# Kernel optimization log

Hardware: AMD Instinct MI355X
Metric: run time of the kernel (lower is better)

Reference implementation:

```python
import jax, jax.numpy as jnp
import numpy as np

DIM = 128
N_NODES = 50000
N_EDGES = 625000


def setup_inputs() -> dict:
    key = jax.random.key(0)
    ks = jax.random.split(key, 6)
    X = jax.random.normal(ks[0], (N_NODES, DIM), dtype=jnp.float32)
    edge_index = jax.random.randint(ks[1], (2, N_EDGES), 0, N_NODES, dtype=jnp.int64)
    # Linear params, init like torch (uniform +/- 1/sqrt(dim))
    bound = 1.0 / np.sqrt(DIM)
    msg_w = jax.random.uniform(ks[2], (DIM, DIM), minval=-bound, maxval=bound, dtype=jnp.float32)
    msg_b = jax.random.uniform(ks[3], (DIM,), minval=-bound, maxval=bound, dtype=jnp.float32)
    lin_w = jax.random.uniform(ks[4], (DIM, DIM), minval=-bound, maxval=bound, dtype=jnp.float32)
    lin_b = jax.random.uniform(ks[5], (DIM,), minval=-bound, maxval=bound, dtype=jnp.float32)
    eps = jnp.asarray(0.0, dtype=jnp.float32)
    return {"X": X, "edge_index": edge_index, "eps": eps,
            "msg_w": msg_w, "msg_b": msg_b, "lin_w": lin_w, "lin_b": lin_b}


def reference(X, edge_index, eps, msg_w, msg_b, lin_w, lin_b):
    src, dst = edge_index[0], edge_index[1]
    # msg_lin(X) then gather at dst: (E, F)
    msg = (jnp.einsum('nf,gf->ng', X, msg_w) + msg_b)[dst]
    # scatter-add messages onto src nodes: (N, F)
    agg = jax.ops.segment_sum(msg, src, num_segments=X.shape[0])
    out = (1.0 + eps) * X + agg
    out = jnp.einsum('nf,gf->ng', out, lin_w) + lin_b
    return jax.nn.relu(out)
```

## Files before the change

### kernel.cpp

```cpp
#include <hip/hip_runtime.h>
#include <hip/hip_bf16.h>

#define NN 50000
#define NE 625000
#define DIM 128

#define NBKT 782
#define NBKTP 784
#define CAP 1536
#define CHUNK 4096
#define NCHUNK ((NE + CHUNK - 1) / CHUNK)

using fragAB = __attribute__((ext_vector_type(8))) short;
using fragC  = __attribute__((ext_vector_type(4))) float;

__device__ __forceinline__ unsigned short f2bf(float f) {
    unsigned int u = __float_as_uint(f);
    unsigned int r = u + 0x7FFFu + ((u >> 16) & 1u);
    return (unsigned short)(r >> 16);
}

__device__ __forceinline__ float bflo(unsigned v) { return __uint_as_float(v << 16); }
__device__ __forceinline__ float bfhi(unsigned v) { return __uint_as_float(v & 0xffff0000u); }

__global__ void prep_kernel(const float* __restrict__ L, const float* __restrict__ W,
                            const float* __restrict__ mb, float* __restrict__ cb,
                            unsigned short* __restrict__ Bh) {
    int idx = blockIdx.x * 256 + threadIdx.x;
    if (idx < DIM * DIM) {
        int o = idx >> 7, g = idx & 127;
        float s = 0.f;
        for (int f = 0; f < DIM; f++) s += L[o * DIM + f] * W[f * DIM + g];
        Bh[o * 256 + 128 + g] = f2bf(s);
        Bh[o * 256 + g] = f2bf(L[o * DIM + g]);
    } else if (idx < DIM * DIM + DIM) {
        int o = idx - DIM * DIM;
        float s = 0.f;
        for (int f = 0; f < DIM; f++) s += L[o * DIM + f] * mb[f];
        cb[o] = s;
    }
}

__global__ __launch_bounds__(256) void xcast_kernel(const float* __restrict__ X,
                                                    unsigned short* __restrict__ Ah) {
    int idx = (blockIdx.x * 256 + threadIdx.x) * 4;
    if (idx >= NN * DIM) return;
    int n = idx >> 7, k = idx & 127;
    float4 v = *(const float4*)(X + idx);
    uint2 p;
    p.x = (unsigned int)f2bf(v.x) | ((unsigned int)f2bf(v.y) << 16);
    p.y = (unsigned int)f2bf(v.z) | ((unsigned int)f2bf(v.w) << 16);
    *(uint2*)(Ah + (size_t)n * 256 + k) = p;
}

__global__ __launch_bounds__(256) void bin_kernel(const int* __restrict__ ei,
                                                  int* __restrict__ bucket_cursor,
                                                  unsigned* __restrict__ staging) {
    __shared__ int cnt[NBKTP];
    __shared__ int base[NBKTP];
    __shared__ int gb[NBKTP];
    __shared__ int sarr[256];
    __shared__ unsigned staged[CHUNK];
    int t = threadIdx.x;
    int e0 = blockIdx.x * CHUNK;
    int nthis = NE - e0; if (nthis > CHUNK) nthis = CHUNK;

    for (int i = t; i < NBKTP; i += 256) cnt[i] = 0;
    __syncthreads();

    unsigned pk[16];
#pragma unroll
    for (int i = 0; i < 16; i++) {
        int e = e0 + i * 256 + t;
        if (e < NE) {
            int s = ei[e];
            int d = ei[NE + e];
            unsigned b = (unsigned)s >> 6;
            pk[i] = (b << 22) | ((unsigned)(s & 63) << 16) | (unsigned)d;
            atomicAdd(&cnt[b], 1);
        } else pk[i] = 0xFFFFFFFFu;
    }
    __syncthreads();

    int myb = t * 4;
    int s0 = 0;
    if (myb < NBKTP) s0 = cnt[myb] + cnt[myb + 1] + cnt[myb + 2] + cnt[myb + 3];
    sarr[t] = s0;
    __syncthreads();
    for (int off = 1; off < 256; off <<= 1) {
        int v = (t >= off) ? sarr[t - off] : 0;
        __syncthreads();
        sarr[t] += v;
        __syncthreads();
    }
    int run = sarr[t] - s0;
    if (myb < NBKTP) {
        for (int i = 0; i < 4; i++) {
            int b = myb + i;
            base[b] = run;
            int c = cnt[b];
            gb[b] = (b < NBKT && c > 0) ? atomicAdd(&bucket_cursor[b], c) : 0;
            run += c;
        }
    }
    __syncthreads();
    if (myb < NBKTP) {
        for (int i = 0; i < 4; i++) cnt[myb + i] = base[myb + i];
    }
    __syncthreads();

#pragma unroll
    for (int i = 0; i < 16; i++) {
        if (pk[i] != 0xFFFFFFFFu) {
            unsigned b = pk[i] >> 22;
            int pos = atomicAdd(&cnt[b], 1);
            staged[pos] = pk[i];
        }
    }
    __syncthreads();

    for (int idx = t; idx < nthis; idx += 256) {
        unsigned p = staged[idx];
        unsigned b = p >> 22;
        int pos = gb[b] + (idx - base[b]);
        if (pos < CAP) staging[(size_t)b * CAP + pos] = p;
    }
}

__global__ __launch_bounds__(256) void bucket_scan(const int* __restrict__ bucket_cursor,
                                                   int* __restrict__ bucket_base) {
    __shared__ int s[256];
    int t = threadIdx.x;
    int myb = t * 4;
    int v[4]; int s0 = 0;
#pragma unroll
    for (int i = 0; i < 4; i++) {
        int b = myb + i;
        int c = (b < NBKT) ? bucket_cursor[b] : 0;
        if (c > CAP) c = CAP;
        v[i] = c; s0 += c;
    }
    s[t] = s0;
    __syncthreads();
    for (int off = 1; off < 256; off <<= 1) {
        int u = (t >= off) ? s[t - off] : 0;
        __syncthreads();
        s[t] += u;
        __syncthreads();
    }
    int run = s[t] - s0;
#pragma unroll
    for (int i = 0; i < 4; i++) {
        int b = myb + i;
        if (b < NBKT) bucket_base[b] = run;
        run += v[i];
    }
}

__global__ __launch_bounds__(256) void bucket_sort(const int* __restrict__ bucket_cursor,
                                                   const int* __restrict__ bucket_base,
                                                   const unsigned* __restrict__ staging,
                                                   int* __restrict__ deg, int* __restrict__ offs,
                                                   int* __restrict__ sdst) {
    __shared__ unsigned rec[CAP];
    __shared__ unsigned sorted_[CAP];
    __shared__ int hcnt[64];
    __shared__ int hbase[64];
    __shared__ int cur[64];
    int t = threadIdx.x;
    int b = blockIdx.x;
    int cnt_b = bucket_cursor[b];
    if (cnt_b > CAP) cnt_b = CAP;
    int base_b = bucket_base[b];

    if (t < 64) hcnt[t] = 0;
    __syncthreads();
    for (int i = t; i < cnt_b; i += 256) {
        unsigned r = staging[(size_t)b * CAP + i];
        rec[i] = r;
        atomicAdd(&hcnt[(r >> 16) & 63], 1);
    }
    __syncthreads();
    if (t == 0) {
        int run = 0;
        for (int i = 0; i < 64; i++) { hbase[i] = run; run += hcnt[i]; }
    }
    __syncthreads();
    if (t < 64) {
        cur[t] = hbase[t];
        int src = b * 64 + t;
        if (src < NN) {
            deg[src] = hcnt[t];
            offs[src] = base_b + hbase[t];
        }
    }
    __syncthreads();
    for (int i = t; i < cnt_b; i += 256) {
        unsigned r = rec[i];
        int pos = atomicAdd(&cur[(r >> 16) & 63], 1);
        sorted_[pos] = r;
    }
    __syncthreads();
    for (int i = t; i < cnt_b; i += 256)
        sdst[base_b + i] = (int)(sorted_[i] & 0xFFFFu);
}

__global__ __launch_bounds__(256) void gather_kernel(const int* __restrict__ offs,
                                                     const int* __restrict__ deg,
                                                     const int* __restrict__ sdst,
                                                     unsigned short* Ah) {
    int wave = (blockIdx.x * 256 + threadIdx.x) >> 6;
    int lane = threadIdx.x & 63;
    if (wave >= NN) return;
    int start = __builtin_amdgcn_readfirstlane(offs[wave]);
    int cnt = __builtin_amdgcn_readfirstlane(deg[wave]);
    const unsigned* __restrict__ Ad = (const unsigned*)Ah;
    float ax = 0.f, ay = 0.f;
    int j = 0;
    for (; j + 8 <= cnt; j += 8) {
        int d0 = sdst[start + j + 0];
        int d1 = sdst[start + j + 1];
        int d2 = sdst[start + j + 2];
        int d3 = sdst[start + j + 3];
        int d4 = sdst[start + j + 4];
        int d5 = sdst[start + j + 5];
        int d6 = sdst[start + j + 6];
        int d7 = sdst[start + j + 7];
        unsigned v0 = Ad[(size_t)d0 * 128 + lane];
        unsigned v1 = Ad[(size_t)d1 * 128 + lane];
        unsigned v2 = Ad[(size_t)d2 * 128 + lane];
        unsigned v3 = Ad[(size_t)d3 * 128 + lane];
        unsigned v4 = Ad[(size_t)d4 * 128 + lane];
        unsigned v5 = Ad[(size_t)d5 * 128 + lane];
        unsigned v6 = Ad[(size_t)d6 * 128 + lane];
        unsigned v7 = Ad[(size_t)d7 * 128 + lane];
        ax += bflo(v0) + bflo(v1) + bflo(v2) + bflo(v3) +
              bflo(v4) + bflo(v5) + bflo(v6) + bflo(v7);
        ay += bfhi(v0) + bfhi(v1) + bfhi(v2) + bfhi(v3) +
              bfhi(v4) + bfhi(v5) + bfhi(v6) + bfhi(v7);
    }
    if (j + 4 <= cnt) {
        int d0 = sdst[start + j + 0];
        int d1 = sdst[start + j + 1];
        int d2 = sdst[start + j + 2];
        int d3 = sdst[start + j + 3];
        unsigned v0 = Ad[(size_t)d0 * 128 + lane];
        unsigned v1 = Ad[(size_t)d1 * 128 + lane];
        unsigned v2 = Ad[(size_t)d2 * 128 + lane];
        unsigned v3 = Ad[(size_t)d3 * 128 + lane];
        ax += bflo(v0) + bflo(v1) + bflo(v2) + bflo(v3);
        ay += bfhi(v0) + bfhi(v1) + bfhi(v2) + bfhi(v3);
        j += 4;
    }
    for (; j < cnt; j++) {
        int d = sdst[start + j];
        unsigned v = Ad[(size_t)d * 128 + lane];
        ax += bflo(v);
        ay += bfhi(v);
    }
    unsigned packed = (unsigned)f2bf(ax) | ((unsigned)f2bf(ay) << 16);
    ((unsigned*)Ah)[(size_t)wave * 128 + 64 + lane] = packed;
}

__global__ __launch_bounds__(256) void outgemm_kernel(
    const unsigned short* Ah, const unsigned short* __restrict__ Bh,
    const int* __restrict__ deg, const float* __restrict__ cb,
    const float* __restrict__ lin_b, const float* __restrict__ epsp, float* out) {
    __shared__ unsigned short As[128 * 40];
    __shared__ unsigned short Bs[128 * 40];
    int tid = threadIdx.x;
    int lane = tid & 63;
    int wave = tid >> 6;
    int m16 = lane & 15;
    int quad = lane >> 4;
    int waveM = (wave & 1) * 64;
    int waveN = (wave >> 1) * 64;
    int r0 = blockIdx.x * 128;
    float scale = 1.0f + *epsp;

    fragC acc[4][4];
#pragma unroll
    for (int i = 0; i < 4; i++)
#pragma unroll
        for (int j = 0; j < 4; j++) acc[i][j] = (fragC){0.f, 0.f, 0.f, 0.f};

    int srow = tid >> 1;
    int shalf = tid & 1;
    int arow = r0 + srow;
    if (arow >= NN) arow = NN - 1;

    for (int kc = 0; kc < 8; kc++) {
        int kb = kc * 32;
        {
            const uint4* gp = (const uint4*)(Ah + (size_t)arow * 256 + kb + shalf * 16);
            uint4 w0 = gp[0];
            uint4 w1 = gp[1];
            uint4* lp = (uint4*)(As + srow * 40 + shalf * 16);
            lp[0] = w0;
            lp[1] = w1;
        }
        {
            const uint4* gp = (const uint4*)(Bh + (size_t)srow * 256 + kb + shalf * 16);
            uint4 w0 = gp[0];
            uint4 w1 = gp[1];
            if (kb < 128) {
                unsigned int* u0 = (unsigned int*)&w0;
                unsigned int* u1 = (unsigned int*)&w1;
#pragma unroll
                for (int q = 0; q < 4; q++) {
                    float lo = __uint_as_float(u0[q] << 16) * scale;
                    float hi = __uint_as_float(u0[q] & 0xffff0000u) * scale;
                    u0[q] = (unsigned int)f2bf(lo) | ((unsigned int)f2bf(hi) << 16);
                    lo = __uint_as_float(u1[q] << 16) * scale;
                    hi = __uint_as_float(u1[q] & 0xffff0000u) * scale;
                    u1[q] = (unsigned int)f2bf(lo) | ((unsigned int)f2bf(hi) << 16);
                }
            }
            uint4* lp = (uint4*)(Bs + srow * 40 + shalf * 16);
            lp[0] = w0;
            lp[1] = w1;
        }
        __syncthreads();

        fragAB a[4], bfr[4];
#pragma unroll
        for (int i = 0; i < 4; i++)
            a[i] = *(const fragAB*)(As + (waveM + i * 16 + m16) * 40 + quad * 8);
#pragma unroll
        for (int j = 0; j < 4; j++)
            bfr[j] = *(const fragAB*)(Bs + (waveN + j * 16 + m16) * 40 + quad * 8);
#pragma unroll
        for (int i = 0; i < 4; i++)
#pragma unroll
            for (int j = 0; j < 4; j++)
                acc[i][j] = __builtin_amdgcn_mfma_f32_16x16x32_bf16(a[i], bfr[j], acc[i][j], 0, 0, 0);
        __syncthreads();
    }

#pragma unroll
    for (int j = 0; j < 4; j++) {
        int col = waveN + j * 16 + m16;
        float cbc = cb[col];
        float lbc = lin_b[col];
#pragma unroll
        for (int i = 0; i < 4; i++) {
            int rbase = r0 + waveM + i * 16 + quad * 4;
#pragma unroll
            for (int r = 0; r < 4; r++) {
                int row = rbase + r;
                if (row < NN) {
                    float dg = (float)deg[row];
                    float v = acc[i][j][r] + dg * cbc + lbc;
                    out[(size_t)row * 128 + col] = fmaxf(v, 0.f);
                }
            }
        }
    }
}

extern "C" void kernel_launch(void* const* d_in, const int* in_sizes, int n_in,
                              void* d_out, int out_size, void* d_ws, size_t ws_size,
                              hipStream_t stream) {
    const float* X = (const float*)d_in[0];
    const int* ei = (const int*)d_in[1];
    const float* epsp = (const float*)d_in[2];
    const float* msg_w = (const float*)d_in[3];
    const float* msg_b = (const float*)d_in[4];
    const float* lin_w = (const float*)d_in[5];
    const float* lin_b = (const float*)d_in[6];
    float* out = (float*)d_out;

    unsigned short* Ah = (unsigned short*)d_out;

    int* bucket_cursor = (int*)d_ws;
    int* bucket_base = bucket_cursor + 800;
    unsigned* staging = (unsigned*)(bucket_base + 800);
    int* deg = (int*)(staging + (size_t)NBKT * CAP);
    int* offs = deg + NN;
    int* sdst = offs + NN;
    float* cb = (float*)(sdst + NE);
    unsigned short* Bh = (unsigned short*)(cb + DIM);

    hipMemsetAsync(bucket_cursor, 0, NBKT * sizeof(int), stream);

    prep_kernel<<<(DIM * DIM + DIM + 255) / 256, 256, 0, stream>>>(lin_w, msg_w, msg_b, cb, Bh);
    xcast_kernel<<<(NN * DIM / 4 + 255) / 256, 256, 0, stream>>>(X, Ah);
    bin_kernel<<<NCHUNK, 256, 0, stream>>>(ei, bucket_cursor, staging);
    bucket_scan<<<1, 256, 0, stream>>>(bucket_cursor, bucket_base);
    bucket_sort<<<NBKT, 256, 0, stream>>>(bucket_cursor, bucket_base, staging, deg, offs, sdst);
    gather_kernel<<<(NN * 64 + 255) / 256, 256, 0, stream>>>(offs, deg, sdst, Ah);
    outgemm_kernel<<<(NN + 127) / 128, 256, 0, stream>>>(Ah, Bh, deg, cb, lin_b, epsp, out);
}
```

Measured before the change: 171.8 us.

## Fuse neighbor gather into output GEMM and drop bucket scan kernel

The per-node neighbor aggregation moves into the GEMM kernel: each block gathers its 128 rows into shared memory and feeds them directly as the second half of the K dimension. This avoids writing and re-reading the aggregated bf16 rows through global memory. The bucket scan kernel is removed by using a fixed per-bucket offset of b*CAP in the sorted edge array, and the binning chunk size is halved to launch more bin blocks. The trade-off is far fewer concurrent waves doing the latency-bound gather, plus extra shared memory per block that lowers occupancy.

```diff
diff --git a/kernel.cpp b/kernel.cpp
--- a/kernel.cpp
+++ b/kernel.cpp
@@ -8,7 +8,7 @@
 #define NBKT 782
 #define NBKTP 784
 #define CAP 1536
-#define CHUNK 4096
+#define CHUNK 2048
 #define NCHUNK ((NE + CHUNK - 1) / CHUNK)
 
 using fragAB = __attribute__((ext_vector_type(8))) short;
@@ -42,15 +42,14 @@
 }
 
 __global__ __launch_bounds__(256) void xcast_kernel(const float* __restrict__ X,
-                                                    unsigned short* __restrict__ Ah) {
+                                                    unsigned short* __restrict__ Xbf) {
     int idx = (blockIdx.x * 256 + threadIdx.x) * 4;
     if (idx >= NN * DIM) return;
-    int n = idx >> 7, k = idx & 127;
     float4 v = *(const float4*)(X + idx);
     uint2 p;
     p.x = (unsigned int)f2bf(v.x) | ((unsigned int)f2bf(v.y) << 16);
     p.y = (unsigned int)f2bf(v.z) | ((unsigned int)f2bf(v.w) << 16);
-    *(uint2*)(Ah + (size_t)n * 256 + k) = p;
+    *(uint2*)(Xbf + idx) = p;
 }
 
 __global__ __launch_bounds__(256) void bin_kernel(const int* __restrict__ ei,
@@ -68,9 +67,9 @@
     for (int i = t; i < NBKTP; i += 256) cnt[i] = 0;
     __syncthreads();
 
-    unsigned pk[16];
-#pragma unroll
-    for (int i = 0; i < 16; i++) {
+    unsigned pk[CHUNK / 256];
+#pragma unroll
+    for (int i = 0; i < CHUNK / 256; i++) {
         int e = e0 + i * 256 + t;
         if (e < NE) {
             int s = ei[e];
@@ -110,7 +109,7 @@
     __syncthreads();
 
 #pragma unroll
-    for (int i = 0; i < 16; i++) {
+    for (int i = 0; i < CHUNK / 256; i++) {
         if (pk[i] != 0xFFFFFFFFu) {
             unsigned b = pk[i] >> 22;
             int pos = atomicAdd(&cnt[b], 1);
@@ -127,38 +126,7 @@
     }
 }
 
-__global__ __launch_bounds__(256) void bucket_scan(const int* __restrict__ bucket_cursor,
-                                                   int* __restrict__ bucket_base) {
-    __shared__ int s[256];
-    int t = threadIdx.x;
-    int myb = t * 4;
-    int v[4]; int s0 = 0;
-#pragma unroll
-    for (int i = 0; i < 4; i++) {
-        int b = myb + i;
-        int c = (b < NBKT) ? bucket_cursor[b] : 0;
-        if (c > CAP) c = CAP;
-        v[i] = c; s0 += c;
-    }
-    s[t] = s0;
-    __syncthreads();
-    for (int off = 1; off < 256; off <<= 1) {
-        int u = (t >= off) ? s[t - off] : 0;
-        __syncthreads();
-        s[t] += u;
-        __syncthreads();
-    }
-    int run = s[t] - s0;
-#pragma unroll
-    for (int i = 0; i < 4; i++) {
-        int b = myb + i;
-        if (b < NBKT) bucket_base[b] = run;
-        run += v[i];
-    }
-}
-
 __global__ __launch_bounds__(256) void bucket_sort(const int* __restrict__ bucket_cursor,
-                                                   const int* __restrict__ bucket_base,
                                                    const unsigned* __restrict__ staging,
                                                    int* __restrict__ deg, int* __restrict__ offs,
                                                    int* __restrict__ sdst) {
@@ -171,7 +139,7 @@
     int b = blockIdx.x;
     int cnt_b = bucket_cursor[b];
     if (cnt_b > CAP) cnt_b = CAP;
-    int base_b = bucket_base[b];
+    int base_b = b * CAP;
 
     if (t < 64) hcnt[t] = 0;
     __syncthreads();
@@ -205,77 +173,80 @@
         sdst[base_b + i] = (int)(sorted_[i] & 0xFFFFu);
 }
 
-__global__ __launch_bounds__(256) void gather_kernel(const int* __restrict__ offs,
-                                                     const int* __restrict__ deg,
-                                                     const int* __restrict__ sdst,
-                                                     unsigned short* Ah) {
-    int wave = (blockIdx.x * 256 + threadIdx.x) >> 6;
-    int lane = threadIdx.x & 63;
-    if (wave >= NN) return;
-    int start = __builtin_amdgcn_readfirstlane(offs[wave]);
-    int cnt = __builtin_amdgcn_readfirstlane(deg[wave]);
-    const unsigned* __restrict__ Ad = (const unsigned*)Ah;
-    float ax = 0.f, ay = 0.f;
-    int j = 0;
-    for (; j + 8 <= cnt; j += 8) {
-        int d0 = sdst[start + j + 0];
-        int d1 = sdst[start + j + 1];
-        int d2 = sdst[start + j + 2];
-        int d3 = sdst[start + j + 3];
-        int d4 = sdst[start + j + 4];
-        int d5 = sdst[start + j + 5];
-        int d6 = sdst[start + j + 6];
-        int d7 = sdst[start + j + 7];
-        unsigned v0 = Ad[(size_t)d0 * 128 + lane];
-        unsigned v1 = Ad[(size_t)d1 * 128 + lane];
-        unsigned v2 = Ad[(size_t)d2 * 128 + lane];
-        unsigned v3 = Ad[(size_t)d3 * 128 + lane];
-        unsigned v4 = Ad[(size_t)d4 * 128 + lane];
-        unsigned v5 = Ad[(size_t)d5 * 128 + lane];
-        unsigned v6 = Ad[(size_t)d6 * 128 + lane];
-        unsigned v7 = Ad[(size_t)d7 * 128 + lane];
-        ax += bflo(v0) + bflo(v1) + bflo(v2) + bflo(v3) +
-              bflo(v4) + bflo(v5) + bflo(v6) + bflo(v7);
-        ay += bfhi(v0) + bfhi(v1) + bfhi(v2) + bfhi(v3) +
-              bfhi(v4) + bfhi(v5) + bfhi(v6) + bfhi(v7);
-    }
-    if (j + 4 <= cnt) {
-        int d0 = sdst[start + j + 0];
-        int d1 = sdst[start + j + 1];
-        int d2 = sdst[start + j + 2];
-        int d3 = sdst[start + j + 3];
-        unsigned v0 = Ad[(size_t)d0 * 128 + lane];
-        unsigned v1 = Ad[(size_t)d1 * 128 + lane];
-        unsigned v2 = Ad[(size_t)d2 * 128 + lane];
-        unsigned v3 = Ad[(size_t)d3 * 128 + lane];
-        ax += bflo(v0) + bflo(v1) + bflo(v2) + bflo(v3);
-        ay += bfhi(v0) + bfhi(v1) + bfhi(v2) + bfhi(v3);
-        j += 4;
-    }
-    for (; j < cnt; j++) {
-        int d = sdst[start + j];
-        unsigned v = Ad[(size_t)d * 128 + lane];
-        ax += bflo(v);
-        ay += bfhi(v);
-    }
-    unsigned packed = (unsigned)f2bf(ax) | ((unsigned)f2bf(ay) << 16);
-    ((unsigned*)Ah)[(size_t)wave * 128 + 64 + lane] = packed;
-}
-
-__global__ __launch_bounds__(256) void outgemm_kernel(
-    const unsigned short* Ah, const unsigned short* __restrict__ Bh,
-    const int* __restrict__ deg, const float* __restrict__ cb,
-    const float* __restrict__ lin_b, const float* __restrict__ epsp, float* out) {
+__global__ __launch_bounds__(256) void fused_kernel(
+    const unsigned short* __restrict__ Xbf, const unsigned short* __restrict__ Bh,
+    const int* __restrict__ deg, const int* __restrict__ offs,
+    const int* __restrict__ sdst, const float* __restrict__ cb,
+    const float* __restrict__ lin_b, const float* __restrict__ epsp,
+    float* __restrict__ out) {
+    __shared__ unsigned short agg[128 * 136];
     __shared__ unsigned short As[128 * 40];
     __shared__ unsigned short Bs[128 * 40];
     int tid = threadIdx.x;
     int lane = tid & 63;
     int wave = tid >> 6;
+    int r0 = blockIdx.x * 128;
+    const unsigned* __restrict__ Xd = (const unsigned*)Xbf;
+
+    for (int i = 0; i < 32; i++) {
+        int lr = wave * 32 + i;
+        int row = r0 + lr;
+        if (row < NN) {
+            int start = __builtin_amdgcn_readfirstlane(offs[row]);
+            int cnt = __builtin_amdgcn_readfirstlane(deg[row]);
+            float ax = 0.f, ay = 0.f;
+            int j = 0;
+            for (; j + 8 <= cnt; j += 8) {
+                int d0 = sdst[start + j + 0];
+                int d1 = sdst[start + j + 1];
+                int d2 = sdst[start + j + 2];
+                int d3 = sdst[start + j + 3];
+                int d4 = sdst[start + j + 4];
+                int d5 = sdst[start + j + 5];
+                int d6 = sdst[start + j + 6];
+                int d7 = sdst[start + j + 7];
+                unsigned v0 = Xd[(size_t)d0 * 64 + lane];
+                unsigned v1 = Xd[(size_t)d1 * 64 + lane];
+                unsigned v2 = Xd[(size_t)d2 * 64 + lane];
+                unsigned v3 = Xd[(size_t)d3 * 64 + lane];
+                unsigned v4 = Xd[(size_t)d4 * 64 + lane];
+                unsigned v5 = Xd[(size_t)d5 * 64 + lane];
+                unsigned v6 = Xd[(size_t)d6 * 64 + lane];
+                unsigned v7 = Xd[(size_t)d7 * 64 + lane];
+                ax += bflo(v0) + bflo(v1) + bflo(v2) + bflo(v3) +
+                      bflo(v4) + bflo(v5) + bflo(v6) + bflo(v7);
+                ay += bfhi(v0) + bfhi(v1) + bfhi(v2) + bfhi(v3) +
+                      bfhi(v4) + bfhi(v5) + bfhi(v6) + bfhi(v7);
+            }
+            if (j + 4 <= cnt) {
+                int d0 = sdst[start + j + 0];
+                int d1 = sdst[start + j + 1];
+                int d2 = sdst[start + j + 2];
+                int d3 = sdst[start + j + 3];
+                unsigned v0 = Xd[(size_t)d0 * 64 + lane];
+                unsigned v1 = Xd[(size_t)d1 * 64 + lane];
+                unsigned v2 = Xd[(size_t)d2 * 64 + lane];
+                unsigned v3 = Xd[(size_t)d3 * 64 + lane];
+                ax += bflo(v0) + bflo(v1) + bflo(v2) + bflo(v3);
+                ay += bfhi(v0) + bfhi(v1) + bfhi(v2) + bfhi(v3);
+                j += 4;
+            }
+            for (; j < cnt; j++) {
+                int d = sdst[start + j];
+                unsigned v = Xd[(size_t)d * 64 + lane];
+                ax += bflo(v);
+                ay += bfhi(v);
+            }
+            ((unsigned*)agg)[lr * 68 + lane] =
+                (unsigned)f2bf(ax) | ((unsigned)f2bf(ay) << 16);
+        }
+    }
+    __syncthreads();
+
     int m16 = lane & 15;
     int quad = lane >> 4;
     int waveM = (wave & 1) * 64;
     int waveN = (wave >> 1) * 64;
-    int r0 = blockIdx.x * 128;
     float scale = 1.0f + *epsp;
 
     fragC acc[4][4];
@@ -291,8 +262,8 @@
 
     for (int kc = 0; kc < 8; kc++) {
         int kb = kc * 32;
-        {
-            const uint4* gp = (const uint4*)(Ah + (size_t)arow * 256 + kb + shalf * 16);
+        if (kc < 4) {
+            const uint4* gp = (const uint4*)(Xbf + (size_t)arow * 128 + kb + shalf * 16);
             uint4 w0 = gp[0];
             uint4 w1 = gp[1];
             uint4* lp = (uint4*)(As + srow * 40 + shalf * 16);
@@ -308,12 +279,12 @@
                 unsigned int* u1 = (unsigned int*)&w1;
 #pragma unroll
                 for (int q = 0; q < 4; q++) {
-                    float lo = __uint_as_float(u0[q] << 16) * scale;
-                    float hi = __uint_as_float(u0[q] & 0xffff0000u) * scale;
-                    u0[q] = (unsigned int)f2bf(lo) | ((unsigned int)f2bf(hi) << 16);
-                    lo = __uint_as_float(u1[q] << 16) * scale;
-                    hi = __uint_as_float(u1[q] & 0xffff0000u) * scale;
-                    u1[q] = (unsigned int)f2bf(lo) | ((unsigned int)f2bf(hi) << 16);
+                    float lo = bflo(u0[q]) * scale;
+                    float hi = bfhi(u0[q]) * scale;
+                    u0[q] = (unsigned)f2bf(lo) | ((unsigned)f2bf(hi) << 16);
+                    lo = bflo(u1[q]) * scale;
+                    hi = bfhi(u1[q]) * scale;
+                    u1[q] = (unsigned)f2bf(lo) | ((unsigned)f2bf(hi) << 16);
                 }
             }
             uint4* lp = (uint4*)(Bs + srow * 40 + shalf * 16);
@@ -324,8 +295,12 @@
 
         fragAB a[4], bfr[4];
 #pragma unroll
-        for (int i = 0; i < 4; i++)
-            a[i] = *(const fragAB*)(As + (waveM + i * 16 + m16) * 40 + quad * 8);
+        for (int i = 0; i < 4; i++) {
+            int r = waveM + i * 16 + m16;
+            a[i] = (kc < 4)
+                ? *(const fragAB*)(As + r * 40 + quad * 8)
+                : *(const fragAB*)(agg + r * 136 + (kb - 128) + quad * 8);
+        }
 #pragma unroll
         for (int j = 0; j < 4; j++)
             bfr[j] = *(const fragAB*)(Bs + (waveN + j * 16 + m16) * 40 + quad * 8);
@@ -370,24 +345,21 @@
     const float* lin_b = (const float*)d_in[6];
     float* out = (float*)d_out;
 
-    unsigned short* Ah = (unsigned short*)d_out;
-
     int* bucket_cursor = (int*)d_ws;
-    int* bucket_base = bucket_cursor + 800;
-    unsigned* staging = (unsigned*)(bucket_base + 800);
-    int* deg = (int*)(staging + (size_t)NBKT * CAP);
+    unsigned* staging = (unsigned*)(bucket_cursor + 800);
+    int* sdst = (int*)(staging + (size_t)NBKT * CAP);
+    int* deg = sdst + (size_t)NBKT * CAP;
     int* offs = deg + NN;
-    int* sdst = offs + NN;
-    float* cb = (float*)(sdst + NE);
+    float* cb = (float*)(offs + NN);
     unsigned short* Bh = (unsigned short*)(cb + DIM);
+    unsigned short* Xbf = Bh + 128 * 256;
 
     hipMemsetAsync(bucket_cursor, 0, NBKT * sizeof(int), stream);
 
     prep_kernel<<<(DIM * DIM + DIM + 255) / 256, 256, 0, stream>>>(lin_w, msg_w, msg_b, cb, Bh);
-    xcast_kernel<<<(NN * DIM / 4 + 255) / 256, 256, 0, stream>>>(X, Ah);
+    xcast_kernel<<<(NN * DIM / 4 + 255) / 256, 256, 0, stream>>>(X, Xbf);
     bin_kernel<<<NCHUNK, 256, 0, stream>>>(ei, bucket_cursor, staging);
-    bucket_scan<<<1, 256, 0, stream>>>(bucket_cursor, bucket_base);
-    bucket_sort<<<NBKT, 256, 0, stream>>>(bucket_cursor, bucket_base, staging, deg, offs, sdst);
-    gather_kernel<<<(NN * 64 + 255) / 256, 256, 0, stream>>>(offs, deg, sdst, Ah);
-    outgemm_kernel<<<(NN + 127) / 128, 256, 0, stream>>>(Ah, Bh, deg, cb, lin_b, epsp, out);
-}
+    bucket_sort<<<NBKT, 256, 0, stream>>>(bucket_cursor, staging, deg, offs, sdst);
+    fused_kernel<<<(NN + 127) / 128, 256, 0, stream>>>(Xbf, Bh, deg, offs, sdst, cb, lin_b,
+                                                       epsp, out);
+}
```

Measured after the change: 207.5 us. 1.21x slower.
